# Performance work log

Hardware: AMD Instinct MI355X
Metric: run time of the kernel (lower is better)

The kernel has to match this reference:

```python
import jax, jax.numpy as jnp
import numpy as np

B, A, N, K, F, E = 2, 5, 1000, 16, 256, 3


def setup_inputs() -> dict:
    key = jax.random.key(0)
    ks = jax.random.split(key, 6)
    nfeature = jax.random.normal(ks[0], (B, A, N, F), dtype=jnp.float32)
    nn_idx = jax.random.randint(ks[1], (B, A, N, K), 0, N)
    etype = jax.random.randint(ks[2], (B, A, N, K), 0, E)
    W = jax.random.normal(ks[3], (A, E, F, F), dtype=jnp.float32) * (1.0 / np.sqrt(F))
    b = jnp.zeros((A, E, F), dtype=jnp.float32)
    W1 = jax.random.normal(ks[4], (A, F, F), dtype=jnp.float32) * (1.0 / np.sqrt(F))
    W2 = jax.random.normal(ks[5], (A, F, F), dtype=jnp.float32) * (1.0 / np.sqrt(F))
    b2 = jnp.zeros((A, F), dtype=jnp.float32)
    return {"nfeature": nfeature, "nn_idx": nn_idx, "etype": etype,
            "W": W, "b": b, "W1": W1, "W2": W2, "b2": b2}


def reference(nfeature, nn_idx, etype, W, b, W1, W2, b2):
    Bs, As, Ns, Fs = nfeature.shape
    Ks = nn_idx.shape[-1]
    Es = W.shape[1]
    # gather neighbor features per anchor: [B, A, N, K, F]
    idx = nn_idx.reshape(Bs, As, Ns * Ks, 1)
    nbr = jnp.take_along_axis(nfeature, idx, axis=2).reshape(Bs, As, Ns, Ks, Fs)
    onehot = jax.nn.one_hot(etype, Es, dtype=nfeature.dtype)  # [B, A, N, K, E]
    # edge-type-specific pointwise transform (loop over small fixed E)
    msg = jnp.zeros((Bs, As, Ns, Ks, Fs), dtype=nfeature.dtype)
    for e in range(Es):
        y = jnp.einsum('bankf,afg->bankg', nbr, W[:, e]) + b[:, e][None, :, None, None, :]
        msg = msg + onehot[..., e:e + 1] * y
    pw = jax.nn.relu(msg.mean(axis=3))  # aggregate over K neighbors -> [B, A, N, F]
    # hop: mix each anchor with the summed 'mutual' feature
    mutual = pw.sum(axis=1)  # [B, N, F]
    hop = jax.nn.relu(jnp.einsum('banf,afg->bang', pw, W1)
                      + jnp.einsum('bnf,afg->bang', mutual, W2)
                      + b2[None, :, None, :])
    return hop + nfeature  # residual add
```

## Files before the change

### kernel.cpp

```cpp
#include <hip/hip_runtime.h>

typedef float f32x4 __attribute__((ext_vector_type(4)));
typedef __bf16 bf16x8 __attribute__((ext_vector_type(8)));
typedef unsigned short u16x4 __attribute__((ext_vector_type(4)));
typedef unsigned short u16x8 __attribute__((ext_vector_type(8)));

constexpr int B_ = 2, A_ = 5, N_ = 1000, K_ = 16, F_ = 256, E_ = 3;
constexpr int RTOT = B_ * N_;
constexpr int ROWS = 2016;
constexpr int TIL  = 32;
constexpr int NT   = ROWS / TIL;
constexpr int GBL  = NT * A_;
constexpr int KS1  = (E_ * F_) / 32;
constexpr int KS2  = (2 * F_) / 32;
constexpr int NTL  = F_ / 16;

constexpr int GATHER_BLOCKS = (A_ * ROWS) / 4;
constexpr int PACK_THREADS  = A_ * KS1 * NTL * 64 + A_ * KS2 * NTL * 64;
constexpr int PACK_BLOCKS   = PACK_THREADS / 256;

constexpr size_t SZ_WPK  = (size_t)A_ * KS1 * NTL * 512 * 2;
constexpr size_t OFF_W12 = SZ_WPK;
constexpr size_t SZ_W12  = (size_t)A_ * KS2 * NTL * 512 * 2;
constexpr size_t OFF_PWB = OFF_W12 + SZ_W12;
constexpr size_t SZ_PWB  = (size_t)A_ * ROWS * F_ * 2;
constexpr size_t OFF_SG  = OFF_PWB + SZ_PWB;
constexpr size_t SZ_SG   = (size_t)A_ * ROWS * (E_ * F_) * 2;
constexpr size_t OFF_CNT = OFF_SG + SZ_SG;

__device__ __forceinline__ unsigned short f2bf(float x) {
  unsigned int u = __builtin_bit_cast(unsigned int, x);
  u += 0x7fffu + ((u >> 16) & 1u);
  return (unsigned short)(u >> 16);
}
__device__ __forceinline__ float bf2f(unsigned short h) {
  return __builtin_bit_cast(float, (unsigned int)h << 16);
}
__device__ __forceinline__ int swz315(int bid) {
  const int xcd = bid & 7, idx = bid >> 3;
  return (xcd < 3 ? xcd * 40 : 120 + (xcd - 3) * 39) + idx;
}

__global__ __launch_bounds__(256) void k_gather_pack(
    const float* __restrict__ nf, const int* __restrict__ nn_idx,
    const int* __restrict__ et, const float* __restrict__ W,
    const float* __restrict__ W1, const float* __restrict__ W2,
    unsigned short* __restrict__ Sg, float* __restrict__ CNTS,
    unsigned short* __restrict__ wpk, unsigned short* __restrict__ w12)
{
  if (blockIdx.x < GATHER_BLOCKS) {
    const int bid  = blockIdx.x;
    const int nbid = (bid & 7) * (GATHER_BLOCKS / 8) + (bid >> 3);
    const int task = nbid * 4 + (threadIdx.x >> 6);
    const int lane = threadIdx.x & 63;
    const int a  = task / ROWS;
    const int rp = task - a * ROWS;
    const int rg = rp < RTOT ? rp : RTOT - 1;
    const int bb = rg / N_;
    const int n  = rg - bb * N_;
    const int eoff = ((bb * A_ + a) * N_ + n) * K_;

    int4 iv[4], ev[4];
#pragma unroll
    for (int q = 0; q < 4; ++q) {
      iv[q] = *reinterpret_cast<const int4*>(nn_idx + eoff + q * 4);
      ev[q] = *reinterpret_cast<const int4*>(et + eoff + q * 4);
    }
    const float* __restrict__ slab =
        nf + (size_t)(bb * A_ + a) * N_ * F_ + lane * 4;
    f32x4 a0 = {0.f, 0.f, 0.f, 0.f}, a1 = a0, a2 = a0;
    int c0 = 0, c1 = 0, c2 = 0;
#pragma unroll
    for (int q = 0; q < 4; ++q) {
#pragma unroll
      for (int j = 0; j < 4; ++j) {
        const int id = ((const int*)&iv[q])[j];
        const int e  = ((const int*)&ev[q])[j];
        const f32x4 v = *reinterpret_cast<const f32x4*>(slab + (size_t)id * F_);
        if (e == 0)      { a0 += v; ++c0; }
        else if (e == 1) { a1 += v; ++c1; }
        else             { a2 += v; ++c2; }
      }
    }
    unsigned short* __restrict__ row = Sg + ((size_t)a * ROWS + rp) * 768;
    const int sw = (rp & 7) << 3;
    u16x4 p0, p1, p2;
#pragma unroll
    for (int j = 0; j < 4; ++j) {
      p0[j] = f2bf(a0[j]); p1[j] = f2bf(a1[j]); p2[j] = f2bf(a2[j]);
    }
    *reinterpret_cast<u16x4*>(row + ((0 * F_ + lane * 4) ^ sw)) = p0;
    *reinterpret_cast<u16x4*>(row + ((1 * F_ + lane * 4) ^ sw)) = p1;
    *reinterpret_cast<u16x4*>(row + ((2 * F_ + lane * 4) ^ sw)) = p2;
    if (lane == 0) {
      f32x4 c = {(float)c0, (float)c1, (float)c2, 0.f};
      *reinterpret_cast<f32x4*>(CNTS + (size_t)task * 4) = c;
    }
  } else {
    const int id = (blockIdx.x - GATHER_BLOCKS) * 256 + threadIdx.x;
    const int T1 = A_ * KS1 * NTL * 64;
    const int T2 = A_ * KS2 * NTL * 64;
    if (id < T1) {
      const int lane = id & 63, nt = (id >> 6) & 15;
      const int r = id >> 10, t = r % KS1, a = r / KS1;
      const int k0 = t * 32 + (lane >> 4) * 8;
      const int n  = nt * 16 + (lane & 15);
      const float* src = W + ((size_t)a * E_ * F_ + k0) * F_ + n;
      u16x8 v;
#pragma unroll
      for (int j = 0; j < 8; ++j) v[j] = f2bf(src[(size_t)j * F_]);
      *reinterpret_cast<u16x8*>(wpk + (size_t)id * 8) = v;
    } else if (id < T1 + T2) {
      const int p = id - T1;
      const int lane = p & 63, nt = (p >> 6) & 15;
      const int r = p >> 10, t = r % KS2, a = r / KS2;
      const int k0 = t * 32 + (lane >> 4) * 8;
      const int n  = nt * 16 + (lane & 15);
      u16x8 v;
#pragma unroll
      for (int j = 0; j < 8; ++j) {
        const int k = k0 + j;
        const float s = (k < F_) ? W1[((size_t)a * F_ + k) * F_ + n]
                                 : W2[((size_t)a * F_ + (k - F_)) * F_ + n];
        v[j] = f2bf(s);
      }
      *reinterpret_cast<u16x8*>(w12 + (size_t)p * 8) = v;
    }
  }
}

__global__ __launch_bounds__(512) void k_gemm1(
    const unsigned short* __restrict__ Sg, const float* __restrict__ CNTS,
    const unsigned short* __restrict__ wpk, const float* __restrict__ bias,
    unsigned short* __restrict__ pwb)
{
  __shared__ alignas(16) unsigned short S[TIL * E_ * F_];
  __shared__ float CNT[TIL][4];
  const int lin = swz315(blockIdx.x);
  const int tq  = lin / A_;
  const int a   = lin - tq * A_;
  const int r0  = tq * TIL;
  const int tid = threadIdx.x;

  const unsigned short* src = Sg + ((size_t)a * ROWS + r0) * 768;
#pragma unroll
  for (int it = 0; it < 6; ++it) {
    const int off = (it * 512 + tid) * 8;
    __builtin_amdgcn_global_load_lds(
        (const __attribute__((address_space(1))) unsigned int*)(src + off),
        (__attribute__((address_space(3))) unsigned int*)(S + off), 16, 0, 0);
  }
  if (tid < TIL)
    *reinterpret_cast<f32x4*>(&CNT[tid][0]) =
        *reinterpret_cast<const f32x4*>(CNTS + (size_t)(a * ROWS + r0 + tid) * 4);
  __syncthreads();

  const int lane = tid & 63, wv = tid >> 6;
  const int arow = lane & 15, kg = lane >> 4;
  const unsigned short* __restrict__ Wp = wpk + (size_t)a * KS1 * NTL * 512;
  f32x4 acc[2][2];
#pragma unroll
  for (int c = 0; c < 2; ++c)
#pragma unroll
    for (int mb = 0; mb < 2; ++mb) acc[c][mb] = (f32x4){0.f, 0.f, 0.f, 0.f};
  const int ssw = (arow & 7) << 3;
#pragma unroll
  for (int t = 0; t < KS1; ++t) {
    bf16x8 af[2];
#pragma unroll
    for (int mb = 0; mb < 2; ++mb) {
      const int si = ((mb * 16 + arow) * 768 + t * 32 + kg * 8) ^ ssw;
      af[mb] = *reinterpret_cast<const bf16x8*>(&S[si]);
    }
#pragma unroll
    for (int c = 0; c < 2; ++c) {
      const int nt = wv * 2 + c;
      const bf16x8 bfr = *reinterpret_cast<const bf16x8*>(
          Wp + ((size_t)(t * NTL + nt) * 64 + lane) * 8);
#pragma unroll
      for (int mb = 0; mb < 2; ++mb)
        acc[c][mb] = __builtin_amdgcn_mfma_f32_16x16x32_bf16(af[mb], bfr, acc[c][mb], 0, 0, 0);
    }
  }

  const float* __restrict__ ba = bias + a * E_ * F_;
#pragma unroll
  for (int c = 0; c < 2; ++c) {
    const int col = (wv * 2 + c) * 16 + arow;
    const float b0 = ba[col], b1 = ba[F_ + col], b2v = ba[2 * F_ + col];
#pragma unroll
    for (int mb = 0; mb < 2; ++mb) {
#pragma unroll
      for (int rr = 0; rr < 4; ++rr) {
        const int row = mb * 16 + kg * 4 + rr;
        const int r   = r0 + row;
        float x = (acc[c][mb][rr] + CNT[row][0] * b0 + CNT[row][1] * b1 +
                   CNT[row][2] * b2v) * (1.0f / K_);
        x = fmaxf(x, 0.f);
        pwb[((size_t)a * ROWS + r) * F_ + (col ^ ((row & 7) << 3))] = f2bf(x);
      }
    }
  }
}

__global__ __launch_bounds__(512) void k_hop_mfma(
    const unsigned short* __restrict__ pwb, const unsigned short* __restrict__ w12,
    const float* __restrict__ b2, const float* __restrict__ nf,
    float* __restrict__ out)
{
  __shared__ alignas(16) unsigned short S2[2 * TIL * F_];
  const int lin = swz315(blockIdx.x);
  const int tq  = lin / A_;
  const int a   = lin - tq * A_;
  const int r0  = tq * TIL;
  const int tid = threadIdx.x;

  const unsigned short* srcP = pwb + ((size_t)a * ROWS + r0) * F_;
#pragma unroll
  for (int it = 0; it < 2; ++it) {
    const int off = (it * 512 + tid) * 8;
    __builtin_amdgcn_global_load_lds(
        (const __attribute__((address_space(1))) unsigned int*)(srcP + off),
        (__attribute__((address_space(3))) unsigned int*)(S2 + off), 16, 0, 0);
  }
#pragma unroll
  for (int it = 0; it < 2; ++it) {
    const int i = (it * 512 + tid) * 8;
    float s[8] = {0.f, 0.f, 0.f, 0.f, 0.f, 0.f, 0.f, 0.f};
#pragma unroll
    for (int a2 = 0; a2 < A_; ++a2) {
      const u16x8 v = *reinterpret_cast<const u16x8*>(
          pwb + ((size_t)a2 * ROWS + r0) * F_ + i);
#pragma unroll
      for (int j = 0; j < 8; ++j) s[j] += bf2f(v[j]);
    }
    u16x8 o;
#pragma unroll
    for (int j = 0; j < 8; ++j) o[j] = f2bf(s[j]);
    *reinterpret_cast<u16x8*>(&S2[TIL * F_ + i]) = o;
  }
  __syncthreads();

  const int lane = tid & 63, wv = tid >> 6;
  const int arow = lane & 15, kg = lane >> 4;
  const unsigned short* __restrict__ Wp = w12 + (size_t)a * KS2 * NTL * 512;
  f32x4 acc[2][2];
#pragma unroll
  for (int c = 0; c < 2; ++c)
#pragma unroll
    for (int mb = 0; mb < 2; ++mb) acc[c][mb] = (f32x4){0.f, 0.f, 0.f, 0.f};
  const int ssw = (arow & 7) << 3;
#pragma unroll
  for (int t = 0; t < KS2; ++t) {
    const int half = t >> 3;
    const int kk   = (t & 7) * 32;
    bf16x8 af[2];
#pragma unroll
    for (int mb = 0; mb < 2; ++mb) {
      const int si = half * (TIL * F_) + (mb * 16 + arow) * F_ + ((kk + kg * 8) ^ ssw);
      af[mb] = *reinterpret_cast<const bf16x8*>(&S2[si]);
    }
#pragma unroll
    for (int c = 0; c < 2; ++c) {
      const int nt = wv * 2 + c;
      const bf16x8 bfr = *reinterpret_cast<const bf16x8*>(
          Wp + ((size_t)(t * NTL + nt) * 64 + lane) * 8);
#pragma unroll
      for (int mb = 0; mb < 2; ++mb)
        acc[c][mb] = __builtin_amdgcn_mfma_f32_16x16x32_bf16(af[mb], bfr, acc[c][mb], 0, 0, 0);
    }
  }

#pragma unroll
  for (int c = 0; c < 2; ++c) {
    const int col = (wv * 2 + c) * 16 + arow;
    const float bb2 = b2[a * F_ + col];
#pragma unroll
    for (int mb = 0; mb < 2; ++mb) {
#pragma unroll
      for (int rr = 0; rr < 4; ++rr) {
        const int row = mb * 16 + kg * 4 + rr;
        const int r   = r0 + row;
        if (r < RTOT) {
          const int bb = r / N_, n = r - bb * N_;
          const size_t o = ((size_t)(bb * A_ + a) * N_ + n) * F_ + col;
          out[o] = fmaxf(acc[c][mb][rr] + bb2, 0.f) + nf[o];
        }
      }
    }
  }
}

extern "C" void kernel_launch(void* const* d_in, const int* in_sizes, int n_in,
                              void* d_out, int out_size, void* d_ws, size_t ws_size,
                              hipStream_t stream)
{
  const float* nf     = (const float*)d_in[0];
  const int*   nn_idx = (const int*)  d_in[1];
  const int*   et     = (const int*)  d_in[2];
  const float* W      = (const float*)d_in[3];
  const float* bias   = (const float*)d_in[4];
  const float* W1     = (const float*)d_in[5];
  const float* W2     = (const float*)d_in[6];
  const float* b2     = (const float*)d_in[7];
  float* out = (float*)d_out;

  unsigned short* wpk  = (unsigned short*)d_ws;
  unsigned short* w12  = (unsigned short*)((char*)d_ws + OFF_W12);
  unsigned short* pwb  = (unsigned short*)((char*)d_ws + OFF_PWB);
  unsigned short* Sg   = (unsigned short*)((char*)d_ws + OFF_SG);
  float*          CNTS = (float*)((char*)d_ws + OFF_CNT);

  k_gather_pack<<<dim3(GATHER_BLOCKS + PACK_BLOCKS), 256, 0, stream>>>(
      nf, nn_idx, et, W, W1, W2, Sg, CNTS, wpk, w12);

  k_gemm1<<<dim3(GBL), 512, 0, stream>>>(Sg, CNTS, wpk, bias, pwb);
  k_hop_mfma<<<dim3(GBL), 512, 0, stream>>>(pwb, w12, b2, nf, out);
}
```

Before: 47.88 us.

## Fuse gemm1 and hop kernels with per-tile atomic flag barrier

Merges the first GEMM and the hop GEMM into one kernel. Blocks that share a row tile meet at a per-tile atomic counter and spin-wait until all anchors have written their pw outputs. This removes one kernel launch boundary and its drain/fill gap, and reuses the shared memory buffer. It adds a memset of the flags, depends on all blocks of a tile being co-resident, and carries a deadlock risk if they are not.

```diff
diff --git a/kernel.cpp b/kernel.cpp
--- a/kernel.cpp
+++ b/kernel.cpp
@@ -27,6 +27,8 @@
 constexpr size_t OFF_SG  = OFF_PWB + SZ_PWB;
 constexpr size_t SZ_SG   = (size_t)A_ * ROWS * (E_ * F_) * 2;
 constexpr size_t OFF_CNT = OFF_SG + SZ_SG;
+constexpr size_t SZ_CNT  = (size_t)A_ * ROWS * 16;
+constexpr size_t OFF_FLG = OFF_CNT + SZ_CNT;
 
 __device__ __forceinline__ unsigned short f2bf(float x) {
   unsigned int u = __builtin_bit_cast(unsigned int, x);
@@ -129,10 +131,12 @@
   }
 }
 
-__global__ __launch_bounds__(512) void k_gemm1(
+__global__ __launch_bounds__(512) void k_gemm_hop(
     const unsigned short* __restrict__ Sg, const float* __restrict__ CNTS,
     const unsigned short* __restrict__ wpk, const float* __restrict__ bias,
-    unsigned short* __restrict__ pwb)
+    unsigned short* __restrict__ pwb, const unsigned short* __restrict__ w12,
+    const float* __restrict__ b2, const float* __restrict__ nf,
+    float* __restrict__ out, unsigned* __restrict__ flags)
 {
   __shared__ alignas(16) unsigned short S[TIL * E_ * F_];
   __shared__ float CNT[TIL][4];
@@ -141,150 +145,152 @@
   const int a   = lin - tq * A_;
   const int r0  = tq * TIL;
   const int tid = threadIdx.x;
-
-  const unsigned short* src = Sg + ((size_t)a * ROWS + r0) * 768;
-#pragma unroll
-  for (int it = 0; it < 6; ++it) {
-    const int off = (it * 512 + tid) * 8;
-    __builtin_amdgcn_global_load_lds(
-        (const __attribute__((address_space(1))) unsigned int*)(src + off),
-        (__attribute__((address_space(3))) unsigned int*)(S + off), 16, 0, 0);
-  }
-  if (tid < TIL)
-    *reinterpret_cast<f32x4*>(&CNT[tid][0]) =
-        *reinterpret_cast<const f32x4*>(CNTS + (size_t)(a * ROWS + r0 + tid) * 4);
-  __syncthreads();
-
   const int lane = tid & 63, wv = tid >> 6;
   const int arow = lane & 15, kg = lane >> 4;
-  const unsigned short* __restrict__ Wp = wpk + (size_t)a * KS1 * NTL * 512;
-  f32x4 acc[2][2];
-#pragma unroll
-  for (int c = 0; c < 2; ++c)
-#pragma unroll
-    for (int mb = 0; mb < 2; ++mb) acc[c][mb] = (f32x4){0.f, 0.f, 0.f, 0.f};
   const int ssw = (arow & 7) << 3;
-#pragma unroll
-  for (int t = 0; t < KS1; ++t) {
-    bf16x8 af[2];
-#pragma unroll
-    for (int mb = 0; mb < 2; ++mb) {
-      const int si = ((mb * 16 + arow) * 768 + t * 32 + kg * 8) ^ ssw;
-      af[mb] = *reinterpret_cast<const bf16x8*>(&S[si]);
-    }
+
+  {
+    const unsigned short* src = Sg + ((size_t)a * ROWS + r0) * 768;
+#pragma unroll
+    for (int it = 0; it < 6; ++it) {
+      const int off = (it * 512 + tid) * 8;
+      __builtin_amdgcn_global_load_lds(
+          (const __attribute__((address_space(1))) unsigned int*)(src + off),
+          (__attribute__((address_space(3))) unsigned int*)(S + off), 16, 0, 0);
+    }
+    if (tid < TIL)
+      *reinterpret_cast<f32x4*>(&CNT[tid][0]) =
+          *reinterpret_cast<const f32x4*>(CNTS + (size_t)(a * ROWS + r0 + tid) * 4);
+    __syncthreads();
+
+    const unsigned short* __restrict__ Wp = wpk + (size_t)a * KS1 * NTL * 512;
+    f32x4 acc[2][2];
+#pragma unroll
+    for (int c = 0; c < 2; ++c)
+#pragma unroll
+      for (int mb = 0; mb < 2; ++mb) acc[c][mb] = (f32x4){0.f, 0.f, 0.f, 0.f};
+#pragma unroll
+    for (int t = 0; t < KS1; ++t) {
+      bf16x8 af[2];
+#pragma unroll
+      for (int mb = 0; mb < 2; ++mb) {
+        const int si = ((mb * 16 + arow) * 768 + t * 32 + kg * 8) ^ ssw;
+        af[mb] = *reinterpret_cast<const bf16x8*>(&S[si]);
+      }
+#pragma unroll
+      for (int c = 0; c < 2; ++c) {
+        const int nt = wv * 2 + c;
+        const bf16x8 bfr = *reinterpret_cast<const bf16x8*>(
+            Wp + ((size_t)(t * NTL + nt) * 64 + lane) * 8);
+#pragma unroll
+        for (int mb = 0; mb < 2; ++mb)
+          acc[c][mb] = __builtin_amdgcn_mfma_f32_16x16x32_bf16(af[mb], bfr, acc[c][mb], 0, 0, 0);
+      }
+    }
+
+    const float* __restrict__ ba = bias + a * E_ * F_;
 #pragma unroll
     for (int c = 0; c < 2; ++c) {
-      const int nt = wv * 2 + c;
-      const bf16x8 bfr = *reinterpret_cast<const bf16x8*>(
-          Wp + ((size_t)(t * NTL + nt) * 64 + lane) * 8);
-#pragma unroll
-      for (int mb = 0; mb < 2; ++mb)
-        acc[c][mb] = __builtin_amdgcn_mfma_f32_16x16x32_bf16(af[mb], bfr, acc[c][mb], 0, 0, 0);
+      const int col = (wv * 2 + c) * 16 + arow;
+      const float b0 = ba[col], b1 = ba[F_ + col], b2v = ba[2 * F_ + col];
+#pragma unroll
+      for (int mb = 0; mb < 2; ++mb) {
+#pragma unroll
+        for (int rr = 0; rr < 4; ++rr) {
+          const int row = mb * 16 + kg * 4 + rr;
+          const int r   = r0 + row;
+          float x = (acc[c][mb][rr] + CNT[row][0] * b0 + CNT[row][1] * b1 +
+                     CNT[row][2] * b2v) * (1.0f / K_);
+          x = fmaxf(x, 0.f);
+          pwb[((size_t)a * ROWS + r) * F_ + (col ^ ((row & 7) << 3))] = f2bf(x);
+        }
+      }
     }
   }
 
-  const float* __restrict__ ba = bias + a * E_ * F_;
-#pragma unroll
-  for (int c = 0; c < 2; ++c) {
-    const int col = (wv * 2 + c) * 16 + arow;
-    const float b0 = ba[col], b1 = ba[F_ + col], b2v = ba[2 * F_ + col];
-#pragma unroll
-    for (int mb = 0; mb < 2; ++mb) {
-#pragma unroll
-      for (int rr = 0; rr < 4; ++rr) {
-        const int row = mb * 16 + kg * 4 + rr;
-        const int r   = r0 + row;
-        float x = (acc[c][mb][rr] + CNT[row][0] * b0 + CNT[row][1] * b1 +
-                   CNT[row][2] * b2v) * (1.0f / K_);
-        x = fmaxf(x, 0.f);
-        pwb[((size_t)a * ROWS + r) * F_ + (col ^ ((row & 7) << 3))] = f2bf(x);
-      }
-    }
-  }
-}
-
-__global__ __launch_bounds__(512) void k_hop_mfma(
-    const unsigned short* __restrict__ pwb, const unsigned short* __restrict__ w12,
-    const float* __restrict__ b2, const float* __restrict__ nf,
-    float* __restrict__ out)
-{
-  __shared__ alignas(16) unsigned short S2[2 * TIL * F_];
-  const int lin = swz315(blockIdx.x);
-  const int tq  = lin / A_;
-  const int a   = lin - tq * A_;
-  const int r0  = tq * TIL;
-  const int tid = threadIdx.x;
-
-  const unsigned short* srcP = pwb + ((size_t)a * ROWS + r0) * F_;
-#pragma unroll
-  for (int it = 0; it < 2; ++it) {
-    const int off = (it * 512 + tid) * 8;
-    __builtin_amdgcn_global_load_lds(
-        (const __attribute__((address_space(1))) unsigned int*)(srcP + off),
-        (__attribute__((address_space(3))) unsigned int*)(S2 + off), 16, 0, 0);
-  }
-#pragma unroll
-  for (int it = 0; it < 2; ++it) {
-    const int i = (it * 512 + tid) * 8;
-    float s[8] = {0.f, 0.f, 0.f, 0.f, 0.f, 0.f, 0.f, 0.f};
-#pragma unroll
-    for (int a2 = 0; a2 < A_; ++a2) {
-      const u16x8 v = *reinterpret_cast<const u16x8*>(
-          pwb + ((size_t)a2 * ROWS + r0) * F_ + i);
-#pragma unroll
-      for (int j = 0; j < 8; ++j) s[j] += bf2f(v[j]);
-    }
-    u16x8 o;
-#pragma unroll
-    for (int j = 0; j < 8; ++j) o[j] = f2bf(s[j]);
-    *reinterpret_cast<u16x8*>(&S2[TIL * F_ + i]) = o;
+  __syncthreads();
+  if (tid == 0) {
+    __threadfence();
+    __hip_atomic_fetch_add(flags + tq, 1u, __ATOMIC_RELEASE,
+                           __HIP_MEMORY_SCOPE_AGENT);
+    while (__hip_atomic_load(flags + tq, __ATOMIC_ACQUIRE,
+                             __HIP_MEMORY_SCOPE_AGENT) < (unsigned)A_) {
+      __builtin_amdgcn_s_sleep(2);
+    }
   }
   __syncthreads();
-
-  const int lane = tid & 63, wv = tid >> 6;
-  const int arow = lane & 15, kg = lane >> 4;
-  const unsigned short* __restrict__ Wp = w12 + (size_t)a * KS2 * NTL * 512;
-  f32x4 acc[2][2];
-#pragma unroll
-  for (int c = 0; c < 2; ++c)
-#pragma unroll
-    for (int mb = 0; mb < 2; ++mb) acc[c][mb] = (f32x4){0.f, 0.f, 0.f, 0.f};
-  const int ssw = (arow & 7) << 3;
-#pragma unroll
-  for (int t = 0; t < KS2; ++t) {
-    const int half = t >> 3;
-    const int kk   = (t & 7) * 32;
-    bf16x8 af[2];
-#pragma unroll
-    for (int mb = 0; mb < 2; ++mb) {
-      const int si = half * (TIL * F_) + (mb * 16 + arow) * F_ + ((kk + kg * 8) ^ ssw);
-      af[mb] = *reinterpret_cast<const bf16x8*>(&S2[si]);
-    }
+  __threadfence();
+
+  {
+    unsigned short* S2 = S;
+    const unsigned short* srcP = pwb + ((size_t)a * ROWS + r0) * F_;
+#pragma unroll
+    for (int it = 0; it < 2; ++it) {
+      const int off = (it * 512 + tid) * 8;
+      __builtin_amdgcn_global_load_lds(
+          (const __attribute__((address_space(1))) unsigned int*)(srcP + off),
+          (__attribute__((address_space(3))) unsigned int*)(S2 + off), 16, 0, 0);
+    }
+#pragma unroll
+    for (int it = 0; it < 2; ++it) {
+      const int i = (it * 512 + tid) * 8;
+      float s[8] = {0.f, 0.f, 0.f, 0.f, 0.f, 0.f, 0.f, 0.f};
+#pragma unroll
+      for (int a2 = 0; a2 < A_; ++a2) {
+        const u16x8 v = *reinterpret_cast<const u16x8*>(
+            pwb + ((size_t)a2 * ROWS + r0) * F_ + i);
+#pragma unroll
+        for (int j = 0; j < 8; ++j) s[j] += bf2f(v[j]);
+      }
+      u16x8 o;
+#pragma unroll
+      for (int j = 0; j < 8; ++j) o[j] = f2bf(s[j]);
+      *reinterpret_cast<u16x8*>(&S2[TIL * F_ + i]) = o;
+    }
+    __syncthreads();
+
+    const unsigned short* __restrict__ Wp = w12 + (size_t)a * KS2 * NTL * 512;
+    f32x4 acc[2][2];
+#pragma unroll
+    for (int c = 0; c < 2; ++c)
+#pragma unroll
+      for (int mb = 0; mb < 2; ++mb) acc[c][mb] = (f32x4){0.f, 0.f, 0.f, 0.f};
+#pragma unroll
+    for (int t = 0; t < KS2; ++t) {
+      const int half = t >> 3;
+      const int kk   = (t & 7) * 32;
+      bf16x8 af[2];
+#pragma unroll
+      for (int mb = 0; mb < 2; ++mb) {
+        const int si = half * (TIL * F_) + (mb * 16 + arow) * F_ + ((kk + kg * 8) ^ ssw);
+        af[mb] = *reinterpret_cast<const bf16x8*>(&S2[si]);
+      }
+#pragma unroll
+      for (int c = 0; c < 2; ++c) {
+        const int nt = wv * 2 + c;
+        const bf16x8 bfr = *reinterpret_cast<const bf16x8*>(
+            Wp + ((size_t)(t * NTL + nt) * 64 + lane) * 8);
+#pragma unroll
+        for (int mb = 0; mb < 2; ++mb)
+          acc[c][mb] = __builtin_amdgcn_mfma_f32_16x16x32_bf16(af[mb], bfr, acc[c][mb], 0, 0, 0);
+      }
+    }
+
 #pragma unroll
     for (int c = 0; c < 2; ++c) {
-      const int nt = wv * 2 + c;
-      const bf16x8 bfr = *reinterpret_cast<const bf16x8*>(
-          Wp + ((size_t)(t * NTL + nt) * 64 + lane) * 8);
-#pragma unroll
-      for (int mb = 0; mb < 2; ++mb)
-        acc[c][mb] = __builtin_amdgcn_mfma_f32_16x16x32_bf16(af[mb], bfr, acc[c][mb], 0, 0, 0);
-    }
-  }
-
-#pragma unroll
-  for (int c = 0; c < 2; ++c) {
-    const int col = (wv * 2 + c) * 16 + arow;
-    const float bb2 = b2[a * F_ + col];
-#pragma unroll
-    for (int mb = 0; mb < 2; ++mb) {
-#pragma unroll
-      for (int rr = 0; rr < 4; ++rr) {
-        const int row = mb * 16 + kg * 4 + rr;
-        const int r   = r0 + row;
-        if (r < RTOT) {
-          const int bb = r / N_, n = r - bb * N_;
-          const size_t o = ((size_t)(bb * A_ + a) * N_ + n) * F_ + col;
-          out[o] = fmaxf(acc[c][mb][rr] + bb2, 0.f) + nf[o];
+      const int col = (wv * 2 + c) * 16 + arow;
+      const float bb2 = b2[a * F_ + col];
+#pragma unroll
+      for (int mb = 0; mb < 2; ++mb) {
+#pragma unroll
+        for (int rr = 0; rr < 4; ++rr) {
+          const int row = mb * 16 + kg * 4 + rr;
+          const int r   = r0 + row;
+          if (r < RTOT) {
+            const int bb = r / N_, n = r - bb * N_;
+            const size_t o = ((size_t)(bb * A_ + a) * N_ + n) * F_ + col;
+            out[o] = fmaxf(acc[c][mb][rr] + bb2, 0.f) + nf[o];
+          }
         }
       }
     }
@@ -310,10 +316,13 @@
   unsigned short* pwb  = (unsigned short*)((char*)d_ws + OFF_PWB);
   unsigned short* Sg   = (unsigned short*)((char*)d_ws + OFF_SG);
   float*          CNTS = (float*)((char*)d_ws + OFF_CNT);
+  unsigned*       flg  = (unsigned*)((char*)d_ws + OFF_FLG);
+
+  hipMemsetAsync((void*)flg, 0, NT * sizeof(unsigned), stream);
 
   k_gather_pack<<<dim3(GATHER_BLOCKS + PACK_BLOCKS), 256, 0, stream>>>(
       nf, nn_idx, et, W, W1, W2, Sg, CNTS, wpk, w12);
 
-  k_gemm1<<<dim3(GBL), 512, 0, stream>>>(Sg, CNTS, wpk, bias, pwb);
-  k_hop_mfma<<<dim3(GBL), 512, 0, stream>>>(pwb, w12, b2, nf, out);
-}
+  k_gemm_hop<<<dim3(GBL), 512, 0, stream>>>(
+      Sg, CNTS, wpk, bias, pwb, w12, b2, nf, out, flg);
+}
```

Result: slower. 120.1 us (+150.8%).
